# Kernel tuning notes

Measured on AMD Instinct MI355X. Metric: run time of the kernel, lower is better.

Reference implementation:

```python
import jax, jax.numpy as jnp
import numpy as np

K = 24  # number of clusters (all ids in [0,K) assumed present per image)
DELTA_VAR = 1.0
DELTA_DIST = 2.0
VAR_W = 1.0
DIST_W = 1.0
REG_W = 1.0


def setup_inputs() -> dict:
    key = jax.random.key(0)
    k1, k2 = jax.random.split(key)
    data = jax.random.normal(k1, (4, 16, 512, 1024), dtype=jnp.float32)
    labels = jax.random.randint(k2, (4, 512, 1024), 0, K, dtype=jnp.int32)
    return {"data": data, "labels": labels}


def reference(data, labels):
    B, D, H, Wd = data.shape
    N = H * Wd
    # [B, N, D] points, [B*N] global segment ids (batch-offset cluster ids)
    X = jnp.transpose(data.reshape(B, D, N), (0, 2, 1)).reshape(B * N, D)
    seg = (labels.reshape(B, N) + jnp.arange(B, dtype=labels.dtype)[:, None] * K).reshape(-1)

    # per-cluster sums and counts -> centers  [B*K, D]
    sums = jax.ops.segment_sum(X, seg, num_segments=B * K)
    counts = jax.ops.segment_sum(jnp.ones((B * N,), X.dtype), seg, num_segments=B * K)
    centers_flat = sums / counts[:, None]
    centers = centers_flat.reshape(B, K, D)
    counts_bk = counts.reshape(B, K)

    # variance term: per-point hinged distance to own cluster center
    c_per_point = centers_flat[seg]                      # [B*N, D]
    pt_dist = jnp.linalg.norm(X - c_per_point, axis=1)   # [B*N]
    hv = jnp.maximum(pt_dist - DELTA_VAR, 0.0) ** 2
    var_per_cluster = jax.ops.segment_sum(hv, seg, num_segments=B * K).reshape(B, K) / counts_bk
    var_sum = var_per_cluster.sum()

    # distance term: pairwise center distances (diagonal kept, as in original,
    # contributing a constant delta_dist**2 per cluster)
    diff = centers[:, :, None, :] - centers[:, None, :, :]     # [B, K, K, D]
    sq = jnp.sum(diff * diff, axis=-1)                         # [B, K, K]
    eye = jnp.eye(K, dtype=bool)[None]
    cdist = jnp.where(eye, 0.0, jnp.sqrt(jnp.where(eye, 1.0, sq)))
    hd = jnp.maximum(DELTA_DIST - cdist, 0.0) ** 2
    dist_sum = hd.sum() / (2.0 * K * (K - 1))

    # regularization: mean center norm per image, summed over batch
    reg_sum = jnp.linalg.norm(centers, axis=2).mean(axis=1).sum()

    loss = (VAR_W * var_sum + DIST_W * dist_sum + REG_W * reg_sum) / B
    return loss
```

## Files before the change

### kernel.cpp

```cpp
#include <hip/hip_runtime.h>
#include <math.h>

#define KC 24
constexpr int D = 16;
constexpr int B = 4;
constexpr int N = 512 * 1024;
constexpr float DELTA_VAR = 1.0f;
constexpr float DELTA_DIST = 2.0f;


__global__ __launch_bounds__(256) void k_sums(const float* __restrict__ data,
                                              const int* __restrict__ labels,
                                              float* __restrict__ g_sums,
                                              float* __restrict__ g_cnt) {
    __shared__ float s_sum[KC * 17];
    __shared__ float s_cnt[KC];
    const int t = threadIdx.x;
    for (int i = t; i < KC * 17; i += 256) s_sum[i] = 0.f;
    if (t < KC) s_cnt[t] = 0.f;
    __syncthreads();

    const int gid = blockIdx.x * 256 + t;
    const int p0  = gid * 4;
    const int b   = p0 >> 19;
    const int n0  = p0 & (N - 1);

    const int4 lab = *(const int4*)(labels + p0);
    const float* dbase = data + (b * D) * (size_t)N + n0;

    for (int d = 0; d < D; ++d) {
        float4 v = *(const float4*)(dbase + d * (size_t)N);
        atomicAdd(&s_sum[lab.x * 17 + d], v.x);
        atomicAdd(&s_sum[lab.y * 17 + d], v.y);
        atomicAdd(&s_sum[lab.z * 17 + d], v.z);
        atomicAdd(&s_sum[lab.w * 17 + d], v.w);
    }
    atomicAdd(&s_cnt[lab.x], 1.f);
    atomicAdd(&s_cnt[lab.y], 1.f);
    atomicAdd(&s_cnt[lab.z], 1.f);
    atomicAdd(&s_cnt[lab.w], 1.f);
    __syncthreads();

    for (int i = t; i < KC * D + KC; i += 256) {
        if (i < KC * D) {
            int c = i >> 4, d = i & 15;
            atomicAdd(&g_sums[(b * KC + c) * D + d], s_sum[c * 17 + d]);
        } else {
            int c = i - KC * D;
            atomicAdd(&g_cnt[b * KC + c], s_cnt[c]);
        }
    }
}

__global__ __launch_bounds__(256) void k_var(const float* __restrict__ data,
                                             const int* __restrict__ labels,
                                             const float* __restrict__ g_sums,
                                             const float* __restrict__ g_cnt,
                                             float* __restrict__ g_hv) {
    __shared__ float s_c[KC * 17];
    __shared__ float s_hv[KC];
    const int t = threadIdx.x;

    const int gid = blockIdx.x * 256 + t;
    const int p0  = gid * 4;
    const int b   = p0 >> 19;
    const int n0  = p0 & (N - 1);

    for (int i = t; i < KC * D; i += 256) {
        int c = i >> 4, d = i & 15;
        s_c[c * 17 + d] = g_sums[(b * KC + c) * D + d] / g_cnt[b * KC + c];
    }
    if (t < KC) s_hv[t] = 0.f;
    __syncthreads();

    const int4 lab = *(const int4*)(labels + p0);
    const float* dbase = data + (b * D) * (size_t)N + n0;

    float sq0 = 0.f, sq1 = 0.f, sq2 = 0.f, sq3 = 0.f;
    for (int d = 0; d < D; ++d) {
        float4 v = *(const float4*)(dbase + d * (size_t)N);
        float t0 = v.x - s_c[lab.x * 17 + d]; sq0 += t0 * t0;
        float t1 = v.y - s_c[lab.y * 17 + d]; sq1 += t1 * t1;
        float t2 = v.z - s_c[lab.z * 17 + d]; sq2 += t2 * t2;
        float t3 = v.w - s_c[lab.w * 17 + d]; sq3 += t3 * t3;
    }
    float h;
    h = fmaxf(sqrtf(sq0) - DELTA_VAR, 0.f); atomicAdd(&s_hv[lab.x], h * h);
    h = fmaxf(sqrtf(sq1) - DELTA_VAR, 0.f); atomicAdd(&s_hv[lab.y], h * h);
    h = fmaxf(sqrtf(sq2) - DELTA_VAR, 0.f); atomicAdd(&s_hv[lab.z], h * h);
    h = fmaxf(sqrtf(sq3) - DELTA_VAR, 0.f); atomicAdd(&s_hv[lab.w], h * h);
    __syncthreads();

    if (t < KC) atomicAdd(&g_hv[b * KC + t], s_hv[t]);
}

__global__ __launch_bounds__(128) void k_final(const float* __restrict__ g_sums,
                                               const float* __restrict__ g_cnt,
                                               const float* __restrict__ g_hv,
                                               float* __restrict__ out) {
    __shared__ float s_c[B * KC * 17];
    __shared__ float s_red[2];
    const int t = threadIdx.x;

    float acc = 0.f;
    if (t < B * KC) {
        float cnt = g_cnt[t];
        float ns = 0.f;
        for (int d = 0; d < D; ++d) {
            float c = g_sums[t * D + d] / cnt;
            s_c[t * 17 + d] = c;
            ns += c * c;
        }
        acc = g_hv[t] / cnt + sqrtf(ns) / (float)KC;
    }
    __syncthreads();

    float dacc = 0.f;
    for (int idx = t; idx < B * KC * KC; idx += 128) {
        int b = idx / (KC * KC);
        int r = idx % (KC * KC);
        int i = r / KC, j = r % KC;
        float hd;
        if (i == j) {
            hd = DELTA_DIST * DELTA_DIST;
        } else {
            const float* ci = &s_c[(b * KC + i) * 17];
            const float* cj = &s_c[(b * KC + j) * 17];
            float sq = 0.f;
            for (int d = 0; d < D; ++d) { float df = ci[d] - cj[d]; sq += df * df; }
            float hh = fmaxf(DELTA_DIST - sqrtf(sq), 0.f);
            hd = hh * hh;
        }
        dacc += hd;
    }
    float total = acc + dacc / (2.f * KC * (KC - 1));

    for (int o = 32; o > 0; o >>= 1) total += __shfl_down(total, o, 64);
    if ((t & 63) == 0) s_red[t >> 6] = total;
    __syncthreads();
    if (t == 0) out[0] = (s_red[0] + s_red[1]) / (float)B;
}

extern "C" void kernel_launch(void* const* d_in, const int* in_sizes, int n_in,
                              void* d_out, int out_size, void* d_ws, size_t ws_size,
                              hipStream_t stream) {
    const float* data  = (const float*)d_in[0];
    const int* labels  = (const int*)d_in[1];
    float* ws = (float*)d_ws;
    float* g_sums = ws;
    float* g_cnt  = ws + B * KC * D;
    float* g_hv   = g_cnt + B * KC;

    hipMemsetAsync(d_ws, 0, (B * KC * D + 2 * B * KC) * sizeof(float), stream);

    const int blocks = (B * N) / (256 * 4);
    k_sums<<<blocks, 256, 0, stream>>>(data, labels, g_sums, g_cnt);
    k_var <<<blocks, 256, 0, stream>>>(data, labels, g_sums, g_cnt, g_hv);
    k_final<<<1, 128, 0, stream>>>(g_sums, g_cnt, g_hv, (float*)d_out);
}
```

Baseline: 373.8 us.

## Replicate shared-memory histograms, use persistent blocks, and batch loads

Both passes now use 8 replicated shared-memory accumulator copies, selected by thread index, to cut LDS atomic contention on the 24 cluster bins. The grid shrinks from 2048 to 1024 blocks, each looping over several 1024-point chunks. This amortizes shared-memory init and global atomic flushes and reduces global atomics. All 16 feature loads are issued before the atomics for more memory-level parallelism. The variance kernel reads centers with float4 LDS loads from a 20-stride padded layout. The cost is higher register and LDS use, which may lower occupancy.

```diff
diff --git a/kernel.cpp b/kernel.cpp
--- a/kernel.cpp
+++ b/kernel.cpp
@@ -8,46 +8,66 @@
 constexpr float DELTA_VAR = 1.0f;
 constexpr float DELTA_DIST = 2.0f;
 
+constexpr int REP = 8;
+constexpr int RS  = KC * 17;
+constexpr int CS  = 33;
+constexpr int BLOCKS = 1024;
+constexpr int ITERS  = (B * N) / (BLOCKS * 256 * 4);
+
 
 __global__ __launch_bounds__(256) void k_sums(const float* __restrict__ data,
                                               const int* __restrict__ labels,
                                               float* __restrict__ g_sums,
                                               float* __restrict__ g_cnt) {
-    __shared__ float s_sum[KC * 17];
-    __shared__ float s_cnt[KC];
+    __shared__ float s_sum[REP * RS];
+    __shared__ float s_cnt[REP * CS];
     const int t = threadIdx.x;
-    for (int i = t; i < KC * 17; i += 256) s_sum[i] = 0.f;
-    if (t < KC) s_cnt[t] = 0.f;
-    __syncthreads();
-
-    const int gid = blockIdx.x * 256 + t;
-    const int p0  = gid * 4;
-    const int b   = p0 >> 19;
-    const int n0  = p0 & (N - 1);
-
-    const int4 lab = *(const int4*)(labels + p0);
-    const float* dbase = data + (b * D) * (size_t)N + n0;
-
-    for (int d = 0; d < D; ++d) {
-        float4 v = *(const float4*)(dbase + d * (size_t)N);
-        atomicAdd(&s_sum[lab.x * 17 + d], v.x);
-        atomicAdd(&s_sum[lab.y * 17 + d], v.y);
-        atomicAdd(&s_sum[lab.z * 17 + d], v.z);
-        atomicAdd(&s_sum[lab.w * 17 + d], v.w);
-    }
-    atomicAdd(&s_cnt[lab.x], 1.f);
-    atomicAdd(&s_cnt[lab.y], 1.f);
-    atomicAdd(&s_cnt[lab.z], 1.f);
-    atomicAdd(&s_cnt[lab.w], 1.f);
+    for (int i = t; i < REP * RS; i += 256) s_sum[i] = 0.f;
+    for (int i = t; i < REP * CS; i += 256) s_cnt[i] = 0.f;
+    __syncthreads();
+
+    const int chunk = blockIdx.x * (256 * 4 * ITERS);
+    const int b     = chunk >> 19;
+    const int rbase = (t & 7) * RS;
+    const int cbase = (t & 7) * CS;
+
+    for (int it = 0; it < ITERS; ++it) {
+        const int p0 = chunk + it * 1024 + t * 4;
+        const int n0 = p0 & (N - 1);
+        const int4 lab = *(const int4*)(labels + p0);
+        const float* dbase = data + (size_t)(b * D) * N + n0;
+
+        float4 v[D];
+#pragma unroll
+        for (int d = 0; d < D; ++d) v[d] = *(const float4*)(dbase + (size_t)d * N);
+
+#pragma unroll
+        for (int d = 0; d < D; ++d) {
+            atomicAdd(&s_sum[rbase + lab.x * 17 + d], v[d].x);
+            atomicAdd(&s_sum[rbase + lab.y * 17 + d], v[d].y);
+            atomicAdd(&s_sum[rbase + lab.z * 17 + d], v[d].z);
+            atomicAdd(&s_sum[rbase + lab.w * 17 + d], v[d].w);
+        }
+        atomicAdd(&s_cnt[cbase + lab.x], 1.f);
+        atomicAdd(&s_cnt[cbase + lab.y], 1.f);
+        atomicAdd(&s_cnt[cbase + lab.z], 1.f);
+        atomicAdd(&s_cnt[cbase + lab.w], 1.f);
+    }
     __syncthreads();
 
     for (int i = t; i < KC * D + KC; i += 256) {
         if (i < KC * D) {
             int c = i >> 4, d = i & 15;
-            atomicAdd(&g_sums[(b * KC + c) * D + d], s_sum[c * 17 + d]);
+            float s = 0.f;
+#pragma unroll
+            for (int r = 0; r < REP; ++r) s += s_sum[r * RS + c * 17 + d];
+            atomicAdd(&g_sums[b * (KC * D) + i], s);
         } else {
             int c = i - KC * D;
-            atomicAdd(&g_cnt[b * KC + c], s_cnt[c]);
+            float s = 0.f;
+#pragma unroll
+            for (int r = 0; r < REP; ++r) s += s_cnt[r * CS + c];
+            atomicAdd(&g_cnt[b * KC + c], s);
         }
     }
 }
@@ -57,41 +77,72 @@
                                              const float* __restrict__ g_sums,
                                              const float* __restrict__ g_cnt,
                                              float* __restrict__ g_hv) {
-    __shared__ float s_c[KC * 17];
-    __shared__ float s_hv[KC];
+    __shared__ float s_c[KC * 20];
+    __shared__ float s_hv[REP * CS];
     const int t = threadIdx.x;
-
-    const int gid = blockIdx.x * 256 + t;
-    const int p0  = gid * 4;
-    const int b   = p0 >> 19;
-    const int n0  = p0 & (N - 1);
+    const int chunk = blockIdx.x * (256 * 4 * ITERS);
+    const int b     = chunk >> 19;
 
     for (int i = t; i < KC * D; i += 256) {
         int c = i >> 4, d = i & 15;
-        s_c[c * 17 + d] = g_sums[(b * KC + c) * D + d] / g_cnt[b * KC + c];
-    }
-    if (t < KC) s_hv[t] = 0.f;
-    __syncthreads();
-
-    const int4 lab = *(const int4*)(labels + p0);
-    const float* dbase = data + (b * D) * (size_t)N + n0;
-
-    float sq0 = 0.f, sq1 = 0.f, sq2 = 0.f, sq3 = 0.f;
-    for (int d = 0; d < D; ++d) {
-        float4 v = *(const float4*)(dbase + d * (size_t)N);
-        float t0 = v.x - s_c[lab.x * 17 + d]; sq0 += t0 * t0;
-        float t1 = v.y - s_c[lab.y * 17 + d]; sq1 += t1 * t1;
-        float t2 = v.z - s_c[lab.z * 17 + d]; sq2 += t2 * t2;
-        float t3 = v.w - s_c[lab.w * 17 + d]; sq3 += t3 * t3;
-    }
-    float h;
-    h = fmaxf(sqrtf(sq0) - DELTA_VAR, 0.f); atomicAdd(&s_hv[lab.x], h * h);
-    h = fmaxf(sqrtf(sq1) - DELTA_VAR, 0.f); atomicAdd(&s_hv[lab.y], h * h);
-    h = fmaxf(sqrtf(sq2) - DELTA_VAR, 0.f); atomicAdd(&s_hv[lab.z], h * h);
-    h = fmaxf(sqrtf(sq3) - DELTA_VAR, 0.f); atomicAdd(&s_hv[lab.w], h * h);
-    __syncthreads();
-
-    if (t < KC) atomicAdd(&g_hv[b * KC + t], s_hv[t]);
+        s_c[c * 20 + d] = g_sums[b * (KC * D) + i] / g_cnt[b * KC + c];
+    }
+    for (int i = t; i < REP * CS; i += 256) s_hv[i] = 0.f;
+    __syncthreads();
+
+    const int cbase = (t & 7) * CS;
+
+    for (int it = 0; it < ITERS; ++it) {
+        const int p0 = chunk + it * 1024 + t * 4;
+        const int n0 = p0 & (N - 1);
+        const int4 lab = *(const int4*)(labels + p0);
+        const float* dbase = data + (size_t)(b * D) * N + n0;
+
+        float4 v[D];
+#pragma unroll
+        for (int d = 0; d < D; ++d) v[d] = *(const float4*)(dbase + (size_t)d * N);
+
+#define HVPT(LBL, COMP) do {                                                 \
+        const float* cp = &s_c[(LBL) * 20];                                  \
+        float4 ca = *(const float4*)(cp);                                    \
+        float4 cb = *(const float4*)(cp + 4);                                \
+        float4 cc = *(const float4*)(cp + 8);                                \
+        float4 cd = *(const float4*)(cp + 12);                               \
+        float sq = 0.f, df;                                                  \
+        df = v[0].COMP  - ca.x; sq += df * df;                               \
+        df = v[1].COMP  - ca.y; sq += df * df;                               \
+        df = v[2].COMP  - ca.z; sq += df * df;                               \
+        df = v[3].COMP  - ca.w; sq += df * df;                               \
+        df = v[4].COMP  - cb.x; sq += df * df;                               \
+        df = v[5].COMP  - cb.y; sq += df * df;                               \
+        df = v[6].COMP  - cb.z; sq += df * df;                               \
+        df = v[7].COMP  - cb.w; sq += df * df;                               \
+        df = v[8].COMP  - cc.x; sq += df * df;                               \
+        df = v[9].COMP  - cc.y; sq += df * df;                               \
+        df = v[10].COMP - cc.z; sq += df * df;                               \
+        df = v[11].COMP - cc.w; sq += df * df;                               \
+        df = v[12].COMP - cd.x; sq += df * df;                               \
+        df = v[13].COMP - cd.y; sq += df * df;                               \
+        df = v[14].COMP - cd.z; sq += df * df;                               \
+        df = v[15].COMP - cd.w; sq += df * df;                               \
+        float h = fmaxf(sqrtf(sq) - DELTA_VAR, 0.f);                         \
+        atomicAdd(&s_hv[cbase + (LBL)], h * h);                              \
+    } while (0)
+
+        HVPT(lab.x, x);
+        HVPT(lab.y, y);
+        HVPT(lab.z, z);
+        HVPT(lab.w, w);
+#undef HVPT
+    }
+    __syncthreads();
+
+    if (t < KC) {
+        float s = 0.f;
+#pragma unroll
+        for (int r = 0; r < REP; ++r) s += s_hv[r * CS + t];
+        atomicAdd(&g_hv[b * KC + t], s);
+    }
 }
 
 __global__ __launch_bounds__(128) void k_final(const float* __restrict__ g_sums,
@@ -153,8 +204,7 @@
 
     hipMemsetAsync(d_ws, 0, (B * KC * D + 2 * B * KC) * sizeof(float), stream);
 
-    const int blocks = (B * N) / (256 * 4);
-    k_sums<<<blocks, 256, 0, stream>>>(data, labels, g_sums, g_cnt);
-    k_var <<<blocks, 256, 0, stream>>>(data, labels, g_sums, g_cnt, g_hv);
+    k_sums<<<BLOCKS, 256, 0, stream>>>(data, labels, g_sums, g_cnt);
+    k_var <<<BLOCKS, 256, 0, stream>>>(data, labels, g_sums, g_cnt, g_hv);
     k_final<<<1, 128, 0, stream>>>(g_sums, g_cnt, g_hv, (float*)d_out);
 }
```

Result: faster. 364.4 us (-2.5%).

## Replicate shared histograms, prefetch loads, and reduce variance via block-wide sums

Applied to the files above, without the earlier changes.

k_sums now spreads its shared-memory atomics across 8 replicated per-cluster accumulators (chosen by thread lane) to cut LDS atomic contention. It merges the replicas before the global atomics and rotates the flush order per block to spread global atomic traffic. Both streaming kernels software-prefetch the next dimension's float4. k_var scales each point's hinge term by the inverse cluster count, so it does a wave-shuffle block reduction with one global atomic into 64 slots instead of per-cluster shared atomics. The cost is more shared memory per block and some summation-order changes.

```diff
diff --git a/kernel.cpp b/kernel.cpp
--- a/kernel.cpp
+++ b/kernel.cpp
@@ -8,47 +8,68 @@
 constexpr float DELTA_VAR = 1.0f;
 constexpr float DELTA_DIST = 2.0f;
 
+constexpr int REP = 8;
+constexpr int RS  = KC * 17;
+constexpr int CS  = 33;
+constexpr int PTS = 1024;
+constexpr int BLOCKS = (B * N) / PTS;
+
 
 __global__ __launch_bounds__(256) void k_sums(const float* __restrict__ data,
                                               const int* __restrict__ labels,
                                               float* __restrict__ g_sums,
                                               float* __restrict__ g_cnt) {
-    __shared__ float s_sum[KC * 17];
-    __shared__ float s_cnt[KC];
+    __shared__ float s_sum[REP * RS];
+    __shared__ float s_cnt[REP * CS];
     const int t = threadIdx.x;
-    for (int i = t; i < KC * 17; i += 256) s_sum[i] = 0.f;
-    if (t < KC) s_cnt[t] = 0.f;
+    for (int i = t; i < REP * RS; i += 256) s_sum[i] = 0.f;
+    for (int i = t; i < REP * CS; i += 256) s_cnt[i] = 0.f;
     __syncthreads();
 
-    const int gid = blockIdx.x * 256 + t;
-    const int p0  = gid * 4;
-    const int b   = p0 >> 19;
-    const int n0  = p0 & (N - 1);
+    const int chunk = blockIdx.x * PTS;
+    const int b     = chunk >> 19;
+    const int n0    = (chunk & (N - 1)) + t * 4;
 
-    const int4 lab = *(const int4*)(labels + p0);
-    const float* dbase = data + (b * D) * (size_t)N + n0;
+    const int4 lab = *(const int4*)(labels + chunk + t * 4);
+    const int rbase = (t & 7) * RS;
+    const int ax = rbase + lab.x * 17;
+    const int ay = rbase + lab.y * 17;
+    const int az = rbase + lab.z * 17;
+    const int aw = rbase + lab.w * 17;
 
+    const float* base = data + (size_t)(b * D) * N + n0;
+    float4 cur = *(const float4*)(base);
+#pragma unroll
     for (int d = 0; d < D; ++d) {
-        float4 v = *(const float4*)(dbase + d * (size_t)N);
-        atomicAdd(&s_sum[lab.x * 17 + d], v.x);
-        atomicAdd(&s_sum[lab.y * 17 + d], v.y);
-        atomicAdd(&s_sum[lab.z * 17 + d], v.z);
-        atomicAdd(&s_sum[lab.w * 17 + d], v.w);
+        float4 nxt;
+        if (d < D - 1) nxt = *(const float4*)(base + (size_t)(d + 1) * N);
+        atomicAdd(&s_sum[ax + d], cur.x);
+        atomicAdd(&s_sum[ay + d], cur.y);
+        atomicAdd(&s_sum[az + d], cur.z);
+        atomicAdd(&s_sum[aw + d], cur.w);
+        cur = nxt;
     }
-    atomicAdd(&s_cnt[lab.x], 1.f);
-    atomicAdd(&s_cnt[lab.y], 1.f);
-    atomicAdd(&s_cnt[lab.z], 1.f);
-    atomicAdd(&s_cnt[lab.w], 1.f);
+    const int cbase = (t & 7) * CS;
+    atomicAdd(&s_cnt[cbase + lab.x], 1.f);
+    atomicAdd(&s_cnt[cbase + lab.y], 1.f);
+    atomicAdd(&s_cnt[cbase + lab.z], 1.f);
+    atomicAdd(&s_cnt[cbase + lab.w], 1.f);
     __syncthreads();
 
-    for (int i = t; i < KC * D + KC; i += 256) {
-        if (i < KC * D) {
-            int c = i >> 4, d = i & 15;
-            atomicAdd(&g_sums[(b * KC + c) * D + d], s_sum[c * 17 + d]);
-        } else {
-            int c = i - KC * D;
-            atomicAdd(&g_cnt[b * KC + c], s_cnt[c]);
-        }
+    const int rot = (blockIdx.x * 131) & 255;
+    for (int i = t; i < KC * D; i += 256) {
+        int j = (i + rot) % (KC * D);
+        int c = j >> 4, d = j & 15;
+        float s = 0.f;
+#pragma unroll
+        for (int r = 0; r < REP; ++r) s += s_sum[r * RS + c * 17 + d];
+        atomicAdd(&g_sums[b * (KC * D) + j], s);
+    }
+    if (t < KC) {
+        float s = 0.f;
+#pragma unroll
+        for (int r = 0; r < REP; ++r) s += s_cnt[r * CS + t];
+        atomicAdd(&g_cnt[b * KC + t], s);
     }
 }
 
@@ -56,47 +77,56 @@
                                              const int* __restrict__ labels,
                                              const float* __restrict__ g_sums,
                                              const float* __restrict__ g_cnt,
-                                             float* __restrict__ g_hv) {
+                                             float* __restrict__ g_varp) {
     __shared__ float s_c[KC * 17];
-    __shared__ float s_hv[KC];
+    __shared__ float s_ic[KC];
+    __shared__ float s_part[4];
     const int t = threadIdx.x;
-
-    const int gid = blockIdx.x * 256 + t;
-    const int p0  = gid * 4;
-    const int b   = p0 >> 19;
-    const int n0  = p0 & (N - 1);
+    const int chunk = blockIdx.x * PTS;
+    const int b     = chunk >> 19;
+    const int n0    = (chunk & (N - 1)) + t * 4;
 
     for (int i = t; i < KC * D; i += 256) {
         int c = i >> 4, d = i & 15;
-        s_c[c * 17 + d] = g_sums[(b * KC + c) * D + d] / g_cnt[b * KC + c];
+        s_c[c * 17 + d] = g_sums[b * (KC * D) + i] / g_cnt[b * KC + c];
     }
-    if (t < KC) s_hv[t] = 0.f;
+    if (t < KC) s_ic[t] = 1.f / g_cnt[b * KC + t];
     __syncthreads();
 
-    const int4 lab = *(const int4*)(labels + p0);
-    const float* dbase = data + (b * D) * (size_t)N + n0;
+    const int4 lab = *(const int4*)(labels + chunk + t * 4);
+    const int ax = lab.x * 17, ay = lab.y * 17, az = lab.z * 17, aw = lab.w * 17;
 
-    float sq0 = 0.f, sq1 = 0.f, sq2 = 0.f, sq3 = 0.f;
+    const float* base = data + (size_t)(b * D) * N + n0;
+    float4 acc = {0.f, 0.f, 0.f, 0.f};
+    float4 cur = *(const float4*)(base);
+#pragma unroll
     for (int d = 0; d < D; ++d) {
-        float4 v = *(const float4*)(dbase + d * (size_t)N);
-        float t0 = v.x - s_c[lab.x * 17 + d]; sq0 += t0 * t0;
-        float t1 = v.y - s_c[lab.y * 17 + d]; sq1 += t1 * t1;
-        float t2 = v.z - s_c[lab.z * 17 + d]; sq2 += t2 * t2;
-        float t3 = v.w - s_c[lab.w * 17 + d]; sq3 += t3 * t3;
+        float4 nxt;
+        if (d < D - 1) nxt = *(const float4*)(base + (size_t)(d + 1) * N);
+        float df;
+        df = cur.x - s_c[ax + d]; acc.x += df * df;
+        df = cur.y - s_c[ay + d]; acc.y += df * df;
+        df = cur.z - s_c[az + d]; acc.z += df * df;
+        df = cur.w - s_c[aw + d]; acc.w += df * df;
+        cur = nxt;
     }
-    float h;
-    h = fmaxf(sqrtf(sq0) - DELTA_VAR, 0.f); atomicAdd(&s_hv[lab.x], h * h);
-    h = fmaxf(sqrtf(sq1) - DELTA_VAR, 0.f); atomicAdd(&s_hv[lab.y], h * h);
-    h = fmaxf(sqrtf(sq2) - DELTA_VAR, 0.f); atomicAdd(&s_hv[lab.z], h * h);
-    h = fmaxf(sqrtf(sq3) - DELTA_VAR, 0.f); atomicAdd(&s_hv[lab.w], h * h);
+    float h, hsum;
+    h = fmaxf(sqrtf(acc.x) - DELTA_VAR, 0.f); hsum  = h * h * s_ic[lab.x];
+    h = fmaxf(sqrtf(acc.y) - DELTA_VAR, 0.f); hsum += h * h * s_ic[lab.y];
+    h = fmaxf(sqrtf(acc.z) - DELTA_VAR, 0.f); hsum += h * h * s_ic[lab.z];
+    h = fmaxf(sqrtf(acc.w) - DELTA_VAR, 0.f); hsum += h * h * s_ic[lab.w];
+
+    for (int o = 32; o > 0; o >>= 1) hsum += __shfl_down(hsum, o, 64);
+    if ((t & 63) == 0) s_part[t >> 6] = hsum;
     __syncthreads();
-
-    if (t < KC) atomicAdd(&g_hv[b * KC + t], s_hv[t]);
+    if (t == 0)
+        atomicAdd(&g_varp[blockIdx.x & 63],
+                  s_part[0] + s_part[1] + s_part[2] + s_part[3]);
 }
 
 __global__ __launch_bounds__(128) void k_final(const float* __restrict__ g_sums,
                                                const float* __restrict__ g_cnt,
-                                               const float* __restrict__ g_hv,
+                                               const float* __restrict__ g_varp,
                                                float* __restrict__ out) {
     __shared__ float s_c[B * KC * 17];
     __shared__ float s_red[2];
@@ -111,8 +141,9 @@
             s_c[t * 17 + d] = c;
             ns += c * c;
         }
-        acc = g_hv[t] / cnt + sqrtf(ns) / (float)KC;
+        acc = sqrtf(ns) / (float)KC;
     }
+    if (t < 64) acc += g_varp[t];
     __syncthreads();
 
     float dacc = 0.f;
@@ -149,12 +180,11 @@
     float* ws = (float*)d_ws;
     float* g_sums = ws;
     float* g_cnt  = ws + B * KC * D;
-    float* g_hv   = g_cnt + B * KC;
+    float* g_varp = g_cnt + B * KC;
 
-    hipMemsetAsync(d_ws, 0, (B * KC * D + 2 * B * KC) * sizeof(float), stream);
+    hipMemsetAsync(d_ws, 0, (B * KC * D + B * KC + 64) * sizeof(float), stream);
 
-    const int blocks = (B * N) / (256 * 4);
-    k_sums<<<blocks, 256, 0, stream>>>(data, labels, g_sums, g_cnt);
-    k_var <<<blocks, 256, 0, stream>>>(data, labels, g_sums, g_cnt, g_hv);
-    k_final<<<1, 128, 0, stream>>>(g_sums, g_cnt, g_hv, (float*)d_out);
+    k_sums<<<BLOCKS, 256, 0, stream>>>(data, labels, g_sums, g_cnt);
+    k_var <<<BLOCKS, 256, 0, stream>>>(data, labels, g_sums, g_cnt, g_varp);
+    k_final<<<1, 128, 0, stream>>>(g_sums, g_cnt, g_varp, (float*)d_out);
 }
```

Result: faster. 356.2 us (-4.7%).
